# Kernel optimization log

Measured on AMD Instinct MI355X. Metric: run time of the kernel, lower is better.

Reference implementation:

```python
import jax, jax.numpy as jnp
import numpy as np

D_MODEL = 1024
NUM_HEADS = 16
HEAD_DIM = D_MODEL // NUM_HEADS
THETA = 10000.0


def _init_linear(key, d_out, d_in):
    sigma = np.sqrt(2.0 / (d_in + d_out))
    w = jax.random.truncated_normal(key, -3.0, 3.0, (d_out, d_in), dtype=jnp.float32)
    return w * sigma


def setup_inputs() -> dict:
    key = jax.random.key(0)
    kh, kq, kk, kv, ko = jax.random.split(key, 5)
    h = jax.random.normal(kh, (2, 2048, D_MODEL), dtype=jnp.float32)
    return {
        "h": h,
        "wq": _init_linear(kq, D_MODEL, D_MODEL),
        "wk": _init_linear(kk, D_MODEL, D_MODEL),
        "wv": _init_linear(kv, D_MODEL, D_MODEL),
        "wo": _init_linear(ko, D_MODEL, D_MODEL),
    }


def _rope(x, pos):
    # x: [B, H, T, dh]; rotate interleaved pairs (..., 2k, 2k+1)
    dh = x.shape[-1]
    freq = THETA ** (-jnp.arange(0, dh // 2, dtype=jnp.float32) / (dh // 2))
    ang = pos[:, None] * freq[None, :]            # [T, dh/2]
    cos, sin = jnp.cos(ang), jnp.sin(ang)
    xr = x.reshape(*x.shape[:-1], dh // 2, 2)
    x0, x1 = xr[..., 0], xr[..., 1]
    out = jnp.stack((cos * x0 - sin * x1, sin * x0 + cos * x1), axis=-1)
    return out.reshape(x.shape)


def reference(h, wq, wk, wv, wo):
    B, T, D = h.shape
    Hn, dh = NUM_HEADS, HEAD_DIM

    def split_heads(x):  # [B,T,D] -> [B,H,T,dh]
        return x.reshape(B, T, Hn, dh).transpose(0, 2, 1, 3)

    Q = split_heads(h @ wq.T)
    K = split_heads(h @ wk.T)
    V = split_heads(h @ wv.T)

    pos = jnp.arange(T, dtype=jnp.float32)
    Q = _rope(Q, pos)
    K = _rope(K, pos)

    scores = jnp.einsum('bhqd,bhkd->bhqk', Q, K) / jnp.sqrt(jnp.float32(dh))
    mask = jnp.tril(jnp.ones((T, T), dtype=bool))
    scores = jnp.where(mask, scores, -jnp.inf)
    attn = jax.nn.softmax(scores, axis=-1)
    out = jnp.einsum('bhqk,bhkd->bhqd', attn, V)   # [B,H,T,dh]
    out = out.transpose(0, 2, 1, 3).reshape(B, T, D)
    return out @ wo.T
```

## Files before the change

### kernel.cpp

```cpp
#include <hip/hip_runtime.h>
#include <math.h>

typedef __bf16 bf16_t;
typedef __bf16 v8bf __attribute__((ext_vector_type(8)));
typedef __bf16 v4bf __attribute__((ext_vector_type(4)));
typedef float  v4f  __attribute__((ext_vector_type(4)));

#define AS1 __attribute__((address_space(1)))
#define AS3 __attribute__((address_space(3)))

static __device__ __forceinline__ void load_lds16(const bf16_t* g, bf16_t* l) {
    __builtin_amdgcn_global_load_lds((AS1 void*)const_cast<bf16_t*>(g),
                                     (AS3 void*)l, 16, 0, 0);
}

static __device__ __forceinline__ void fast_sincos(float ang, float* sn, float* cs) {
    float rv = ang * 0.15915494309189535f;
    rv -= floorf(rv);
    const float a = rv * 6.283185307179586f;
    *sn = __sinf(a);
    *cs = __cosf(a);
}

__global__ __launch_bounds__(256) void cvt_fp32_bf16(
    const float* __restrict__ h,  const float* __restrict__ wq,
    const float* __restrict__ wk, const float* __restrict__ wv,
    const float* __restrict__ wo,
    bf16_t* __restrict__ hb,  bf16_t* __restrict__ wqb,
    bf16_t* __restrict__ wkb, bf16_t* __restrict__ wvb,
    bf16_t* __restrict__ wob)
{
    const size_t HM = (size_t)4 << 20;
    const size_t i8 = ((size_t)blockIdx.x * 256 + threadIdx.x) * 8;
    const float* src; bf16_t* dst; size_t off;
    if (i8 < HM) { src = h; dst = hb; off = i8; }
    else {
        const size_t r = (i8 - HM) >> 20;
        off = (i8 - HM) & (((size_t)1 << 20) - 1);
        src = (r == 0) ? wq  : (r == 1) ? wk  : (r == 2) ? wv  : wo;
        dst = (r == 0) ? wqb : (r == 1) ? wkb : (r == 2) ? wvb : wob;
    }
    const float4 a = *(const float4*)(src + off);
    const float4 b = *(const float4*)(src + off + 4);
    v8bf o;
    o[0]=(bf16_t)a.x; o[1]=(bf16_t)a.y; o[2]=(bf16_t)a.z; o[3]=(bf16_t)a.w;
    o[4]=(bf16_t)b.x; o[5]=(bf16_t)b.y; o[6]=(bf16_t)b.z; o[7]=(bf16_t)b.w;
    *(v8bf*)(dst + off) = o;
}

__global__ __launch_bounds__(256) void qkv_gemm_rope(
    const bf16_t* __restrict__ A,
    const bf16_t* __restrict__ wq,
    const bf16_t* __restrict__ wk,
    const bf16_t* __restrict__ wv,
    bf16_t* __restrict__ qo, bf16_t* __restrict__ ko, bf16_t* __restrict__ vo)
{
    __shared__ __align__(16) bf16_t smem[17408];
    bf16_t* As = smem;
    bf16_t* Bs = smem + 4096;

    const int tid = threadIdx.x;
    const int n0  = blockIdx.x * 128;
    const int m0  = blockIdx.y * 128;
    const int sel = n0 >> 10;
    const bf16_t* W = (sel == 0) ? wq : (sel == 1) ? wk : wv;
    const int wr0 = n0 & 1023;

    const int wave = tid >> 6;
    const int lane = tid & 63;
    const int l16  = lane & 15;
    const int quad = lane >> 4;
    const int wrow = (wave >> 1) * 64;
    const int wcol = (wave & 1) * 64;

    v4f acc[4][4];
    #pragma unroll
    for (int i = 0; i < 4; ++i)
        #pragma unroll
        for (int j = 0; j < 4; ++j) acc[i][j] = (v4f)(0.0f);

    for (int kt = 0; kt < 32; ++kt) {
        const int k0 = kt * 32;
        #pragma unroll
        for (int rep = 0; rep < 2; ++rep) {
            const int c   = rep * 256 + tid;
            const int row = c >> 2;
            const int col = (c & 3) * 8;
            load_lds16(A + (size_t)(m0 + row) * 1024 + k0 + col, &As[c * 8]);
            load_lds16(W + (size_t)(wr0 + row) * 1024 + k0 + col, &Bs[c * 8]);
        }
        __syncthreads();

        v8bf af[4], bfb[4];
        #pragma unroll
        for (int i = 0; i < 4; ++i) {
            af[i]  = *(const v8bf*)&As[(wrow + i * 16 + l16) * 32 + quad * 8];
            bfb[i] = *(const v8bf*)&Bs[(wcol + i * 16 + l16) * 32 + quad * 8];
        }
        #pragma unroll
        for (int i = 0; i < 4; ++i)
            #pragma unroll
            for (int j = 0; j < 4; ++j)
                acc[i][j] = __builtin_amdgcn_mfma_f32_16x16x32_bf16(
                    af[i], bfb[j], acc[i][j], 0, 0, 0);
        __syncthreads();
    }

    bf16_t* Ls = smem + wave * 4352;
    const int bq     = (m0 + wrow) >> 11;
    const int hd     = ((n0 + wcol) >> 6) & 15;
    const int t_base = (m0 + wrow) & 2047;

    if (sel < 2) {
        bf16_t* OUT = (sel == 0) ? qo : ko;
        #pragma unroll
        for (int i = 0; i < 4; ++i) {
            #pragma unroll
            for (int j = 0; j < 4; ++j) {
                #pragma unroll
                for (int r = 0; r < 4; ++r) {
                    const int mrow = i * 16 + quad * 4 + r;
                    const int dcol = j * 16 + l16;
                    float v = acc[i][j][r];
                    const float vp = __shfl_xor(v, 1);
                    const int t  = t_base + mrow;
                    const int kk = dcol >> 1;
                    const float freq = exp2f((float)kk * -0.4152410118609203f);
                    float sn, cs;
                    fast_sincos((float)t * freq, &sn, &cs);
                    v = ((dcol & 1) == 0) ? (cs * v - sn * vp) : (sn * vp + cs * v);
                    Ls[mrow * 68 + dcol] = (bf16_t)v;
                }
            }
        }
        #pragma unroll
        for (int s = 0; s < 8; ++s) {
            const int row = s * 8 + (lane >> 3);
            const int off = (lane & 7) * 8;
            const v8bf vv = *(const v8bf*)&Ls[row * 68 + off];
            *(v8bf*)(OUT + (((size_t)(bq * 16 + hd) * 2048) + t_base + row) * 64 + off) = vv;
        }
    } else {
        #pragma unroll
        for (int i = 0; i < 4; ++i)
            #pragma unroll
            for (int j = 0; j < 4; ++j) {
                v4bf p;
                #pragma unroll
                for (int r = 0; r < 4; ++r) p[r] = (bf16_t)acc[i][j][r];
                *(v4bf*)&Ls[(j * 16 + l16) * 68 + i * 16 + quad * 4] = p;
            }
        #pragma unroll
        for (int s = 0; s < 8; ++s) {
            const int drow = s * 8 + (lane >> 3);
            const int off  = (lane & 7) * 8;
            const v8bf vv = *(const v8bf*)&Ls[drow * 68 + off];
            *(v8bf*)(vo + (((size_t)(bq * 16 + hd) * 64) + drow) * 2048 + t_base + off) = vv;
        }
    }
}

__global__ __launch_bounds__(512, 4) void attn_mfma(
    const bf16_t* __restrict__ qg,
    const bf16_t* __restrict__ kg,
    const bf16_t* __restrict__ vtg,
    bf16_t* __restrict__ og)
{
    __shared__ __align__(16) bf16_t Ks[2][64 * 72];
    __shared__ __align__(16) bf16_t Vs[2][64 * 72];
    __shared__ __align__(16) bf16_t Ps[8][16 * 72];

    const int tid  = threadIdx.x;
    const int wave = tid >> 6;
    const int lane = tid & 63;
    const int l16  = lane & 15;
    const int quad = lane >> 4;

    const int i  = blockIdx.x;
    const int tt = i >> 3;
    const int u  = tt & 15;
    const int g  = tt >> 4;
    const int q128 = (((g + 1) >> 1) & 1) ? (15 - u) : u;
    const int bh = (i & 7) * 4 + g;
    const int b = bh >> 4, hh = bh & 15;

    const bf16_t* Kb = kg  + (size_t)bh * 2048 * 64;
    const bf16_t* Vb = vtg + (size_t)bh * 64 * 2048;

    const int qglb = q128 * 128 + wave * 16 + l16;
    const int diag_kt = 2 * q128 + (wave >> 2);
    const int ktmax = 2 * q128 + 1;

    const bf16_t* qrow = qg + ((size_t)bh * 2048 + qglb) * 64;
    v8bf qf[2];
    qf[0] = *(const v8bf*)(qrow + quad * 8);
    qf[1] = *(const v8bf*)(qrow + 32 + quad * 8);
    #pragma unroll
    for (int e = 0; e < 8; ++e) {
        qf[0][e] = (bf16_t)((float)qf[0][e] * 0.18033688011112042f);
        qf[1][e] = (bf16_t)((float)qf[1][e] * 0.18033688011112042f);
    }

    v8bf ones1;
    #pragma unroll
    for (int e = 0; e < 8; ++e) ones1[e] = (bf16_t)1.0f;

    float m_r = -1e30f;
    v4f l_acc = (v4f)(0.0f);
    v4f o_acc[4];
    #pragma unroll
    for (int d = 0; d < 4; ++d) o_acc[d] = (v4f)(0.0f);

    const int srow = tid >> 3;
    const int scol = (tid & 7) * 8;
    {
        const v8bf k0 = *(const v8bf*)(Kb + (size_t)srow * 64 + scol);
        const v8bf v0 = *(const v8bf*)(Vb + (size_t)srow * 2048 + scol);
        *(v8bf*)&Ks[0][srow * 72 + scol] = k0;
        *(v8bf*)&Vs[0][srow * 72 + scol] = v0;
    }

    for (int kt = 0; kt <= ktmax; ++kt) {
        const int cur = kt & 1;
        const int nxt = cur ^ 1;
        __syncthreads();

        v8bf kreg, vreg;
        if (kt < ktmax) {
            kreg = *(const v8bf*)(Kb + ((size_t)(kt + 1) * 64 + srow) * 64 + scol);
            vreg = *(const v8bf*)(Vb + (size_t)srow * 2048 + (kt + 1) * 64 + scol);
        }

        const bool active = (kt * 64) <= (q128 * 128 + wave * 16 + 15);
        if (active) {
            v4f s_acc[4];
            #pragma unroll
            for (int kblk = 0; kblk < 4; ++kblk) s_acc[kblk] = (v4f)(0.0f);
            #pragma unroll
            for (int kblk = 0; kblk < 4; ++kblk) {
                const v8bf kf0 = *(const v8bf*)&Ks[cur][(kblk * 16 + l16) * 72 + quad * 8];
                const v8bf kf1 = *(const v8bf*)&Ks[cur][(kblk * 16 + l16) * 72 + 32 + quad * 8];
                s_acc[kblk] = __builtin_amdgcn_mfma_f32_16x16x32_bf16(
                    kf0, qf[0], s_acc[kblk], 0, 0, 0);
                s_acc[kblk] = __builtin_amdgcn_mfma_f32_16x16x32_bf16(
                    kf1, qf[1], s_acc[kblk], 0, 0, 0);
            }

            if (kt == diag_kt) {
                #pragma unroll
                for (int kblk = 0; kblk < 4; ++kblk)
                    #pragma unroll
                    for (int r = 0; r < 4; ++r)
                        if (kt * 64 + kblk * 16 + quad * 4 + r > qglb)
                            s_acc[kblk][r] = -1e30f;
            }

            float mx = -1e30f;
            #pragma unroll
            for (int kblk = 0; kblk < 4; ++kblk)
                #pragma unroll
                for (int r = 0; r < 4; ++r) mx = fmaxf(mx, s_acc[kblk][r]);
            mx = fmaxf(mx, __shfl_xor(mx, 16));
            mx = fmaxf(mx, __shfl_xor(mx, 32));
            const float m_new = fmaxf(m_r, mx);
            const float alpha = exp2f(m_r - m_new);
            m_r = m_new;
            #pragma unroll
            for (int kblk = 0; kblk < 4; ++kblk)
                #pragma unroll
                for (int r = 0; r < 4; ++r)
                    s_acc[kblk][r] = exp2f(s_acc[kblk][r] - m_new);

            #pragma unroll
            for (int kblk = 0; kblk < 4; ++kblk) {
                v4bf p;
                #pragma unroll
                for (int r = 0; r < 4; ++r) p[r] = (bf16_t)s_acc[kblk][r];
                *(v4bf*)&Ps[wave][l16 * 72 + kblk * 16 + quad * 4] = p;
            }
            #pragma unroll
            for (int d = 0; d < 4; ++d) o_acc[d] *= alpha;
            l_acc *= alpha;

            const v8bf pf0 = *(const v8bf*)&Ps[wave][l16 * 72 + quad * 8];
            const v8bf pf1 = *(const v8bf*)&Ps[wave][l16 * 72 + 32 + quad * 8];
            #pragma unroll
            for (int dblk = 0; dblk < 4; ++dblk) {
                const v8bf vf0 = *(const v8bf*)&Vs[cur][(dblk * 16 + l16) * 72 + quad * 8];
                const v8bf vf1 = *(const v8bf*)&Vs[cur][(dblk * 16 + l16) * 72 + 32 + quad * 8];
                o_acc[dblk] = __builtin_amdgcn_mfma_f32_16x16x32_bf16(
                    vf0, pf0, o_acc[dblk], 0, 0, 0);
                o_acc[dblk] = __builtin_amdgcn_mfma_f32_16x16x32_bf16(
                    vf1, pf1, o_acc[dblk], 0, 0, 0);
            }
            l_acc = __builtin_amdgcn_mfma_f32_16x16x32_bf16(ones1, pf0, l_acc, 0, 0, 0);
            l_acc = __builtin_amdgcn_mfma_f32_16x16x32_bf16(ones1, pf1, l_acc, 0, 0, 0);
        }

        if (kt < ktmax) {
            *(v8bf*)&Ks[nxt][srow * 72 + scol] = kreg;
            *(v8bf*)&Vs[nxt][srow * 72 + scol] = vreg;
        }
    }

    const float inv_l = 1.0f / l_acc[0];
    const size_t base = ((size_t)b * 2048 + qglb) * 1024 + hh * 64;
    #pragma unroll
    for (int dblk = 0; dblk < 4; ++dblk) {
        v4bf o;
        #pragma unroll
        for (int r = 0; r < 4; ++r) o[r] = (bf16_t)(o_acc[dblk][r] * inv_l);
        *(v4bf*)(og + base + dblk * 16 + quad * 4) = o;
    }
}

__global__ __launch_bounds__(256) void out_gemm(
    const bf16_t* __restrict__ A,
    const bf16_t* __restrict__ W,
    float* __restrict__ C)
{
    __shared__ __align__(16) float smemf[4352];
    bf16_t* As = (bf16_t*)smemf;
    bf16_t* Bs = As + 4096;

    const int tid = threadIdx.x;
    const int n0  = blockIdx.x * 64;
    const int m0  = blockIdx.y * 128;

    const int wave = tid >> 6;
    const int lane = tid & 63;
    const int l16  = lane & 15;
    const int quad = lane >> 4;
    const int wrow = (wave >> 1) * 64;
    const int wcol = (wave & 1) * 32;

    v4f acc[4][2];
    #pragma unroll
    for (int i = 0; i < 4; ++i)
        #pragma unroll
        for (int j = 0; j < 2; ++j) acc[i][j] = (v4f)(0.0f);

    for (int kt = 0; kt < 32; ++kt) {
        const int k0 = kt * 32;
        #pragma unroll
        for (int rep = 0; rep < 2; ++rep) {
            const int c   = rep * 256 + tid;
            const int row = c >> 2;
            const int col = (c & 3) * 8;
            load_lds16(A + (size_t)(m0 + row) * 1024 + k0 + col, &As[c * 8]);
        }
        {
            const int row = tid >> 2;
            const int col = (tid & 3) * 8;
            load_lds16(W + (size_t)(n0 + row) * 1024 + k0 + col, &Bs[tid * 8]);
        }
        __syncthreads();

        v8bf af[4], bfb[2];
        #pragma unroll
        for (int i = 0; i < 4; ++i)
            af[i]  = *(const v8bf*)&As[(wrow + i * 16 + l16) * 32 + quad * 8];
        #pragma unroll
        for (int j = 0; j < 2; ++j)
            bfb[j] = *(const v8bf*)&Bs[(wcol + j * 16 + l16) * 32 + quad * 8];
        #pragma unroll
        for (int i = 0; i < 4; ++i)
            #pragma unroll
            for (int j = 0; j < 2; ++j)
                acc[i][j] = __builtin_amdgcn_mfma_f32_16x16x32_bf16(
                    af[i], bfb[j], acc[i][j], 0, 0, 0);
        __syncthreads();
    }

    float* Lw = smemf + wave * 1088;
    #pragma unroll
    for (int half = 0; half < 2; ++half) {
        #pragma unroll
        for (int ii = 0; ii < 2; ++ii) {
            const int i = half * 2 + ii;
            #pragma unroll
            for (int j = 0; j < 2; ++j)
                #pragma unroll
                for (int r = 0; r < 4; ++r)
                    Lw[(ii * 16 + quad * 4 + r) * 34 + j * 16 + l16] = acc[i][j][r];
        }
        #pragma unroll
        for (int s = 0; s < 8; ++s) {
            const int row = s * 4 + (lane >> 4);
            const float2 vv = *(const float2*)&Lw[row * 34 + l16 * 2];
            *(float2*)(C + (size_t)(m0 + wrow + half * 32 + row) * 1024
                         + n0 + wcol + l16 * 2) = vv;
        }
    }
}

extern "C" void kernel_launch(void* const* d_in, const int* in_sizes, int n_in,
                              void* d_out, int out_size, void* d_ws, size_t ws_size,
                              hipStream_t stream) {
    const float* h  = (const float*)d_in[0];
    const float* wq = (const float*)d_in[1];
    const float* wk = (const float*)d_in[2];
    const float* wv = (const float*)d_in[3];
    const float* wo = (const float*)d_in[4];

    const size_t NH = (size_t)4096 * 1024;
    const size_t NW = (size_t)1024 * 1024;

    bf16_t* hb  = (bf16_t*)d_ws;
    bf16_t* wqb = hb  + NH;
    bf16_t* wkb = wqb + NW;
    bf16_t* wvb = wkb + NW;
    bf16_t* wob = wvb + NW;
    bf16_t* qw  = wob + NW;
    bf16_t* kw  = qw + NH;
    bf16_t* vw  = kw + NH;
    bf16_t* og  = hb;

    cvt_fp32_bf16<<<dim3(4096), dim3(256), 0, stream>>>(
        h, wq, wk, wv, wo, hb, wqb, wkb, wvb, wob);
    qkv_gemm_rope<<<dim3(24, 32), dim3(256), 0, stream>>>(
        hb, wqb, wkb, wvb, qw, kw, vw);
    attn_mfma<<<dim3(512), dim3(512), 0, stream>>>(qw, kw, vw, og);
    out_gemm<<<dim3(16, 32), dim3(256), 0, stream>>>(og, wob, (float*)d_out);
}
```

Before: 184.8 us.

## Give each attention wave two query tiles, swizzle LDS, skip rescales lazily

```diff
diff --git a/kernel.cpp b/kernel.cpp
--- a/kernel.cpp
+++ b/kernel.cpp
@@ -160,15 +160,15 @@
     }
 }
 
-__global__ __launch_bounds__(512, 4) void attn_mfma(
+__global__ __launch_bounds__(256, 3) void attn_mfma(
     const bf16_t* __restrict__ qg,
     const bf16_t* __restrict__ kg,
     const bf16_t* __restrict__ vtg,
     bf16_t* __restrict__ og)
 {
-    __shared__ __align__(16) bf16_t Ks[2][64 * 72];
-    __shared__ __align__(16) bf16_t Vs[2][64 * 72];
-    __shared__ __align__(16) bf16_t Ps[8][16 * 72];
+    __shared__ __align__(16) bf16_t Ks[2][4096];
+    __shared__ __align__(16) bf16_t Vs[2][4096];
+    __shared__ __align__(16) bf16_t Ps[8][1024];
 
     const int tid  = threadIdx.x;
     const int wave = tid >> 6;
@@ -179,138 +179,193 @@
     const int i  = blockIdx.x;
     const int tt = i >> 3;
     const int u  = tt & 15;
-    const int g  = tt >> 4;
-    const int q128 = (((g + 1) >> 1) & 1) ? (15 - u) : u;
-    const int bh = (i & 7) * 4 + g;
+    const int g4 = tt >> 4;
+    const int q128 = (((g4 + 1) >> 1) & 1) ? (15 - u) : u;
+    const int bh = (i & 7) * 4 + g4;
     const int b = bh >> 4, hh = bh & 15;
 
     const bf16_t* Kb = kg  + (size_t)bh * 2048 * 64;
     const bf16_t* Vb = vtg + (size_t)bh * 64 * 2048;
 
-    const int qglb = q128 * 128 + wave * 16 + l16;
-    const int diag_kt = 2 * q128 + (wave >> 2);
-    const int ktmax = 2 * q128 + 1;
-
-    const bf16_t* qrow = qg + ((size_t)bh * 2048 + qglb) * 64;
-    v8bf qf[2];
-    qf[0] = *(const v8bf*)(qrow + quad * 8);
-    qf[1] = *(const v8bf*)(qrow + 32 + quad * 8);
-    #pragma unroll
-    for (int e = 0; e < 8; ++e) {
-        qf[0][e] = (bf16_t)((float)qf[0][e] * 0.18033688011112042f);
-        qf[1][e] = (bf16_t)((float)qf[1][e] * 0.18033688011112042f);
+    const int qrow0   = q128 * 128 + wave * 32;
+    const int ktmax_w = 2 * q128 + (wave >> 1);
+    const int ktmax_b = 2 * q128 + 1;
+
+    const int sw  = (l16 & 7) << 4;
+    const int cb0 = (quad << 4) ^ sw;
+
+    v8bf qf[2][2];
+    #pragma unroll
+    for (int g = 0; g < 2; ++g) {
+        const bf16_t* qrow = qg + ((size_t)bh * 2048 + qrow0 + g * 16 + l16) * 64;
+        qf[g][0] = *(const v8bf*)(qrow + quad * 8);
+        qf[g][1] = *(const v8bf*)(qrow + 32 + quad * 8);
+        #pragma unroll
+        for (int e = 0; e < 8; ++e) {
+            qf[g][0][e] = (bf16_t)((float)qf[g][0][e] * 0.18033688011112042f);
+            qf[g][1][e] = (bf16_t)((float)qf[g][1][e] * 0.18033688011112042f);
+        }
     }
 
     v8bf ones1;
     #pragma unroll
     for (int e = 0; e < 8; ++e) ones1[e] = (bf16_t)1.0f;
 
-    float m_r = -1e30f;
-    v4f l_acc = (v4f)(0.0f);
-    v4f o_acc[4];
-    #pragma unroll
-    for (int d = 0; d < 4; ++d) o_acc[d] = (v4f)(0.0f);
-
-    const int srow = tid >> 3;
-    const int scol = (tid & 7) * 8;
+    float m_r[2] = {-1e30f, -1e30f};
+    v4f l_acc[2];
+    l_acc[0] = (v4f)(0.0f); l_acc[1] = (v4f)(0.0f);
+    v4f o_acc[2][4];
+    #pragma unroll
+    for (int g = 0; g < 2; ++g)
+        #pragma unroll
+        for (int d = 0; d < 4; ++d) o_acc[g][d] = (v4f)(0.0f);
+
+    const int srow = tid >> 2;
+    const int sc   = (tid & 3) << 4;
+    const int swr  = (srow & 7) << 4;
+    const int sb0  = (sc * 2) ^ swr;
+    const int sb1  = (sc * 2 + 16) ^ swr;
+
     {
-        const v8bf k0 = *(const v8bf*)(Kb + (size_t)srow * 64 + scol);
-        const v8bf v0 = *(const v8bf*)(Vb + (size_t)srow * 2048 + scol);
-        *(v8bf*)&Ks[0][srow * 72 + scol] = k0;
-        *(v8bf*)&Vs[0][srow * 72 + scol] = v0;
-    }
-
-    for (int kt = 0; kt <= ktmax; ++kt) {
+        const bf16_t* kp = Kb + (size_t)srow * 64 + sc;
+        const bf16_t* vp = Vb + (size_t)srow * 2048 + sc;
+        char* kd = (char*)Ks[0] + (srow << 7);
+        char* vd = (char*)Vs[0] + (srow << 7);
+        *(v8bf*)(kd + sb0) = *(const v8bf*)kp;
+        *(v8bf*)(kd + sb1) = *(const v8bf*)(kp + 8);
+        *(v8bf*)(vd + sb0) = *(const v8bf*)vp;
+        *(v8bf*)(vd + sb1) = *(const v8bf*)(vp + 8);
+    }
+
+    for (int kt = 0; kt <= ktmax_b; ++kt) {
         const int cur = kt & 1;
         const int nxt = cur ^ 1;
         __syncthreads();
 
-        v8bf kreg, vreg;
-        if (kt < ktmax) {
-            kreg = *(const v8bf*)(Kb + ((size_t)(kt + 1) * 64 + srow) * 64 + scol);
-            vreg = *(const v8bf*)(Vb + (size_t)srow * 2048 + (kt + 1) * 64 + scol);
-        }
-
-        const bool active = (kt * 64) <= (q128 * 128 + wave * 16 + 15);
-        if (active) {
-            v4f s_acc[4];
-            #pragma unroll
-            for (int kblk = 0; kblk < 4; ++kblk) s_acc[kblk] = (v4f)(0.0f);
+        v8bf k0, k1, v0, v1;
+        if (kt < ktmax_b) {
+            const bf16_t* kp = Kb + ((size_t)(kt + 1) * 64 + srow) * 64 + sc;
+            const bf16_t* vp = Vb + (size_t)srow * 2048 + (kt + 1) * 64 + sc;
+            k0 = *(const v8bf*)kp; k1 = *(const v8bf*)(kp + 8);
+            v0 = *(const v8bf*)vp; v1 = *(const v8bf*)(vp + 8);
+        }
+
+        if (kt <= ktmax_w) {
+            const char* ksc = (const char*)Ks[cur];
+            v4f s[2][4];
+            #pragma unroll
+            for (int g = 0; g < 2; ++g)
+                #pragma unroll
+                for (int kblk = 0; kblk < 4; ++kblk) s[g][kblk] = (v4f)(0.0f);
             #pragma unroll
             for (int kblk = 0; kblk < 4; ++kblk) {
-                const v8bf kf0 = *(const v8bf*)&Ks[cur][(kblk * 16 + l16) * 72 + quad * 8];
-                const v8bf kf1 = *(const v8bf*)&Ks[cur][(kblk * 16 + l16) * 72 + 32 + quad * 8];
-                s_acc[kblk] = __builtin_amdgcn_mfma_f32_16x16x32_bf16(
-                    kf0, qf[0], s_acc[kblk], 0, 0, 0);
-                s_acc[kblk] = __builtin_amdgcn_mfma_f32_16x16x32_bf16(
-                    kf1, qf[1], s_acc[kblk], 0, 0, 0);
-            }
-
-            if (kt == diag_kt) {
+                const char* kr = ksc + ((kblk * 16 + l16) << 7);
+                const v8bf kf0 = *(const v8bf*)(kr + cb0);
+                const v8bf kf1 = *(const v8bf*)(kr + (cb0 ^ 64));
+                s[0][kblk] = __builtin_amdgcn_mfma_f32_16x16x32_bf16(
+                    kf0, qf[0][0], s[0][kblk], 0, 0, 0);
+                s[1][kblk] = __builtin_amdgcn_mfma_f32_16x16x32_bf16(
+                    kf0, qf[1][0], s[1][kblk], 0, 0, 0);
+                s[0][kblk] = __builtin_amdgcn_mfma_f32_16x16x32_bf16(
+                    kf1, qf[0][1], s[0][kblk], 0, 0, 0);
+                s[1][kblk] = __builtin_amdgcn_mfma_f32_16x16x32_bf16(
+                    kf1, qf[1][1], s[1][kblk], 0, 0, 0);
+            }
+
+            if (kt == ktmax_w) {
+                #pragma unroll
+                for (int g = 0; g < 2; ++g) {
+                    const int qglb = qrow0 + g * 16 + l16;
+                    #pragma unroll
+                    for (int kblk = 0; kblk < 4; ++kblk)
+                        #pragma unroll
+                        for (int r = 0; r < 4; ++r)
+                            if (kt * 64 + kblk * 16 + quad * 4 + r > qglb)
+                                s[g][kblk][r] = -1e30f;
+                }
+            }
+
+            #pragma unroll
+            for (int g = 0; g < 2; ++g) {
+                float mx = -1e30f;
                 #pragma unroll
                 for (int kblk = 0; kblk < 4; ++kblk)
                     #pragma unroll
+                    for (int r = 0; r < 4; ++r) mx = fmaxf(mx, s[g][kblk][r]);
+                mx = fmaxf(mx, __shfl_xor(mx, 16));
+                mx = fmaxf(mx, __shfl_xor(mx, 32));
+                if (!__all(mx - m_r[g] <= 8.0f)) {
+                    const float mn = fmaxf(m_r[g], mx);
+                    const float a  = exp2f(m_r[g] - mn);
+                    m_r[g] = mn;
+                    l_acc[g] *= a;
+                    #pragma unroll
+                    for (int d = 0; d < 4; ++d) o_acc[g][d] *= a;
+                }
+                char* psc = (char*)Ps[wave * 2 + g] + (l16 << 7);
+                #pragma unroll
+                for (int kblk = 0; kblk < 4; ++kblk) {
+                    v4bf p;
+                    #pragma unroll
                     for (int r = 0; r < 4; ++r)
-                        if (kt * 64 + kblk * 16 + quad * 4 + r > qglb)
-                            s_acc[kblk][r] = -1e30f;
-            }
-
-            float mx = -1e30f;
-            #pragma unroll
-            for (int kblk = 0; kblk < 4; ++kblk)
-                #pragma unroll
-                for (int r = 0; r < 4; ++r) mx = fmaxf(mx, s_acc[kblk][r]);
-            mx = fmaxf(mx, __shfl_xor(mx, 16));
-            mx = fmaxf(mx, __shfl_xor(mx, 32));
-            const float m_new = fmaxf(m_r, mx);
-            const float alpha = exp2f(m_r - m_new);
-            m_r = m_new;
-            #pragma unroll
-            for (int kblk = 0; kblk < 4; ++kblk)
-                #pragma unroll
-                for (int r = 0; r < 4; ++r)
-                    s_acc[kblk][r] = exp2f(s_acc[kblk][r] - m_new);
-
-            #pragma unroll
-            for (int kblk = 0; kblk < 4; ++kblk) {
-                v4bf p;
-                #pragma unroll
-                for (int r = 0; r < 4; ++r) p[r] = (bf16_t)s_acc[kblk][r];
-                *(v4bf*)&Ps[wave][l16 * 72 + kblk * 16 + quad * 4] = p;
-            }
-            #pragma unroll
-            for (int d = 0; d < 4; ++d) o_acc[d] *= alpha;
-            l_acc *= alpha;
-
-            const v8bf pf0 = *(const v8bf*)&Ps[wave][l16 * 72 + quad * 8];
-            const v8bf pf1 = *(const v8bf*)&Ps[wave][l16 * 72 + 32 + quad * 8];
+                        p[r] = (bf16_t)exp2f(s[g][kblk][r] - m_r[g]);
+                    *(v4bf*)(psc + (((kblk << 5) + (quad << 3)) ^ sw)) = p;
+                }
+            }
+
+            const char* vsc = (const char*)Vs[cur];
+            v8bf pf[2][2];
+            #pragma unroll
+            for (int g = 0; g < 2; ++g) {
+                const char* psc = (const char*)Ps[wave * 2 + g] + (l16 << 7);
+                pf[g][0] = *(const v8bf*)(psc + cb0);
+                pf[g][1] = *(const v8bf*)(psc + (cb0 ^ 64));
+            }
             #pragma unroll
             for (int dblk = 0; dblk < 4; ++dblk) {
-                const v8bf vf0 = *(const v8bf*)&Vs[cur][(dblk * 16 + l16) * 72 + quad * 8];
-                const v8bf vf1 = *(const v8bf*)&Vs[cur][(dblk * 16 + l16) * 72 + 32 + quad * 8];
-                o_acc[dblk] = __builtin_amdgcn_mfma_f32_16x16x32_bf16(
-                    vf0, pf0, o_acc[dblk], 0, 0, 0);
-                o_acc[dblk] = __builtin_amdgcn_mfma_f32_16x16x32_bf16(
-                    vf1, pf1, o_acc[dblk], 0, 0, 0);
-            }
-            l_acc = __builtin_amdgcn_mfma_f32_16x16x32_bf16(ones1, pf0, l_acc, 0, 0, 0);
-            l_acc = __builtin_amdgcn_mfma_f32_16x16x32_bf16(ones1, pf1, l_acc, 0, 0, 0);
-        }
-
-        if (kt < ktmax) {
-            *(v8bf*)&Ks[nxt][srow * 72 + scol] = kreg;
-            *(v8bf*)&Vs[nxt][srow * 72 + scol] = vreg;
-        }
-    }
-
-    const float inv_l = 1.0f / l_acc[0];
-    const size_t base = ((size_t)b * 2048 + qglb) * 1024 + hh * 64;
-    #pragma unroll
-    for (int dblk = 0; dblk < 4; ++dblk) {
-        v4bf o;
-        #pragma unroll
-        for (int r = 0; r < 4; ++r) o[r] = (bf16_t)(o_acc[dblk][r] * inv_l);
-        *(v4bf*)(og + base + dblk * 16 + quad * 4) = o;
+                const char* vr = vsc + ((dblk * 16 + l16) << 7);
+                const v8bf vf0 = *(const v8bf*)(vr + cb0);
+                const v8bf vf1 = *(const v8bf*)(vr + (cb0 ^ 64));
+                o_acc[0][dblk] = __builtin_amdgcn_mfma_f32_16x16x32_bf16(
+                    vf0, pf[0][0], o_acc[0][dblk], 0, 0, 0);
+                o_acc[1][dblk] = __builtin_amdgcn_mfma_f32_16x16x32_bf16(
+                    vf0, pf[1][0], o_acc[1][dblk], 0, 0, 0);
+                o_acc[0][dblk] = __builtin_amdgcn_mfma_f32_16x16x32_bf16(
+                    vf1, pf[0][1], o_acc[0][dblk], 0, 0, 0);
+                o_acc[1][dblk] = __builtin_amdgcn_mfma_f32_16x16x32_bf16(
+                    vf1, pf[1][1], o_acc[1][dblk], 0, 0, 0);
+            }
+            l_acc[0] = __builtin_amdgcn_mfma_f32_16x16x32_bf16(
+                ones1, pf[0][0], l_acc[0], 0, 0, 0);
+            l_acc[0] = __builtin_amdgcn_mfma_f32_16x16x32_bf16(
+                ones1, pf[0][1], l_acc[0], 0, 0, 0);
+            l_acc[1] = __builtin_amdgcn_mfma_f32_16x16x32_bf16(
+                ones1, pf[1][0], l_acc[1], 0, 0, 0);
+            l_acc[1] = __builtin_amdgcn_mfma_f32_16x16x32_bf16(
+                ones1, pf[1][1], l_acc[1], 0, 0, 0);
+        }
+
+        if (kt < ktmax_b) {
+            char* kd = (char*)Ks[nxt] + (srow << 7);
+            char* vd = (char*)Vs[nxt] + (srow << 7);
+            *(v8bf*)(kd + sb0) = k0;
+            *(v8bf*)(kd + sb1) = k1;
+            *(v8bf*)(vd + sb0) = v0;
+            *(v8bf*)(vd + sb1) = v1;
+        }
+    }
+
+    #pragma unroll
+    for (int g = 0; g < 2; ++g) {
+        const float inv_l = 1.0f / l_acc[g][0];
+        const size_t base = ((size_t)b * 2048 + qrow0 + g * 16 + l16) * 1024 + hh * 64;
+        #pragma unroll
+        for (int dblk = 0; dblk < 4; ++dblk) {
+            v4bf o;
+            #pragma unroll
+            for (int r = 0; r < 4; ++r) o[r] = (bf16_t)(o_acc[g][dblk][r] * inv_l);
+            *(v4bf*)(og + base + dblk * 16 + quad * 4) = o;
+        }
     }
 }
 
@@ -420,6 +475,6 @@
         h, wq, wk, wv, wo, hb, wqb, wkb, wvb, wob);
     qkv_gemm_rope<<<dim3(24, 32), dim3(256), 0, stream>>>(
         hb, wqb, wkb, wvb, qw, kw, vw);
-    attn_mfma<<<dim3(512), dim3(512), 0, stream>>>(qw, kw, vw, og);
+    attn_mfma<<<dim3(512), dim3(256), 0, stream>>>(qw, kw, vw, og);
     out_gemm<<<dim3(16, 32), dim3(256), 0, stream>>>(og, wob, (float*)d_out);
 }
```

Measured after the change: 191.7 us. 1.04x slower.

## Restructure attention: 64-row query tiles, async LDS loads, XOR swizzle, lazy rescale

Applied to the files above, without the earlier changes.

```diff
diff --git a/kernel.cpp b/kernel.cpp
--- a/kernel.cpp
+++ b/kernel.cpp
@@ -11,6 +11,10 @@
 
 static __device__ __forceinline__ void load_lds16(const bf16_t* g, bf16_t* l) {
     __builtin_amdgcn_global_load_lds((AS1 void*)const_cast<bf16_t*>(g),
+                                     (AS3 void*)l, 16, 0, 0);
+}
+static __device__ __forceinline__ void load_lds16b(const char* g, char* l) {
+    __builtin_amdgcn_global_load_lds((AS1 void*)const_cast<char*>(g),
                                      (AS3 void*)l, 16, 0, 0);
 }
 
@@ -160,15 +164,15 @@
     }
 }
 
-__global__ __launch_bounds__(512, 4) void attn_mfma(
+__global__ __launch_bounds__(256, 4) void attn_mfma(
     const bf16_t* __restrict__ qg,
     const bf16_t* __restrict__ kg,
     const bf16_t* __restrict__ vtg,
     bf16_t* __restrict__ og)
 {
-    __shared__ __align__(16) bf16_t Ks[2][64 * 72];
-    __shared__ __align__(16) bf16_t Vs[2][64 * 72];
-    __shared__ __align__(16) bf16_t Ps[8][16 * 72];
+    __shared__ __align__(16) bf16_t Ks[2][4096];
+    __shared__ __align__(16) bf16_t Vs[2][4096];
+    __shared__ __align__(16) bf16_t Ps[4][1024];
 
     const int tid  = threadIdx.x;
     const int wave = tid >> 6;
@@ -176,20 +180,25 @@
     const int l16  = lane & 15;
     const int quad = lane >> 4;
 
-    const int i  = blockIdx.x;
-    const int tt = i >> 3;
-    const int u  = tt & 15;
-    const int g  = tt >> 4;
-    const int q128 = (((g + 1) >> 1) & 1) ? (15 - u) : u;
-    const int bh = (i & 7) * 4 + g;
+    const int i   = blockIdx.x;
+    const int xcd = i & 7;
+    const int j   = i >> 3;
+    const int bhl = j >> 5;
+    const int u   = j & 31;
+    const int q64 = (bhl & 1) ? (31 - u) : u;
+    const int bh  = xcd * 4 + bhl;
     const int b = bh >> 4, hh = bh & 15;
 
-    const bf16_t* Kb = kg  + (size_t)bh * 2048 * 64;
-    const bf16_t* Vb = vtg + (size_t)bh * 64 * 2048;
-
-    const int qglb = q128 * 128 + wave * 16 + l16;
-    const int diag_kt = 2 * q128 + (wave >> 2);
-    const int ktmax = 2 * q128 + 1;
+    const char* Kb = (const char*)(kg  + (size_t)bh * 2048 * 64);
+    const char* Vb = (const char*)(vtg + (size_t)bh * 64 * 2048);
+
+    const int qglb = q64 * 64 + wave * 16 + l16;
+
+    const int sw  = (l16 & 7) << 4;
+    const int cb0 = (quad << 4) ^ sw;
+
+    const int grow = tid >> 3;
+    const int gsw  = ((tid & 7) << 4) ^ ((grow & 7) << 4);
 
     const bf16_t* qrow = qg + ((size_t)bh * 2048 + qglb) * 64;
     v8bf qf[2];
@@ -211,96 +220,98 @@
     #pragma unroll
     for (int d = 0; d < 4; ++d) o_acc[d] = (v4f)(0.0f);
 
-    const int srow = tid >> 3;
-    const int scol = (tid & 7) * 8;
     {
-        const v8bf k0 = *(const v8bf*)(Kb + (size_t)srow * 64 + scol);
-        const v8bf v0 = *(const v8bf*)(Vb + (size_t)srow * 2048 + scol);
-        *(v8bf*)&Ks[0][srow * 72 + scol] = k0;
-        *(v8bf*)&Vs[0][srow * 72 + scol] = v0;
-    }
-
-    for (int kt = 0; kt <= ktmax; ++kt) {
+        const char* ks = Kb + ((size_t)grow << 7) + gsw;
+        const char* vs = Vb + ((size_t)grow << 12) + gsw;
+        char* kd = (char*)Ks[0] + tid * 16;
+        char* vd = (char*)Vs[0] + tid * 16;
+        load_lds16b(ks, kd);
+        load_lds16b(ks + (32 << 7), kd + 4096);
+        load_lds16b(vs, vd);
+        load_lds16b(vs + ((size_t)32 << 12), vd + 4096);
+    }
+
+    for (int kt = 0; kt <= q64; ++kt) {
         const int cur = kt & 1;
         const int nxt = cur ^ 1;
         __syncthreads();
 
-        v8bf kreg, vreg;
-        if (kt < ktmax) {
-            kreg = *(const v8bf*)(Kb + ((size_t)(kt + 1) * 64 + srow) * 64 + scol);
-            vreg = *(const v8bf*)(Vb + (size_t)srow * 2048 + (kt + 1) * 64 + scol);
-        }
-
-        const bool active = (kt * 64) <= (q128 * 128 + wave * 16 + 15);
-        if (active) {
-            v4f s_acc[4];
-            #pragma unroll
-            for (int kblk = 0; kblk < 4; ++kblk) s_acc[kblk] = (v4f)(0.0f);
-            #pragma unroll
-            for (int kblk = 0; kblk < 4; ++kblk) {
-                const v8bf kf0 = *(const v8bf*)&Ks[cur][(kblk * 16 + l16) * 72 + quad * 8];
-                const v8bf kf1 = *(const v8bf*)&Ks[cur][(kblk * 16 + l16) * 72 + 32 + quad * 8];
-                s_acc[kblk] = __builtin_amdgcn_mfma_f32_16x16x32_bf16(
-                    kf0, qf[0], s_acc[kblk], 0, 0, 0);
-                s_acc[kblk] = __builtin_amdgcn_mfma_f32_16x16x32_bf16(
-                    kf1, qf[1], s_acc[kblk], 0, 0, 0);
-            }
-
-            if (kt == diag_kt) {
-                #pragma unroll
-                for (int kblk = 0; kblk < 4; ++kblk)
-                    #pragma unroll
-                    for (int r = 0; r < 4; ++r)
-                        if (kt * 64 + kblk * 16 + quad * 4 + r > qglb)
-                            s_acc[kblk][r] = -1e30f;
-            }
-
-            float mx = -1e30f;
-            #pragma unroll
-            for (int kblk = 0; kblk < 4; ++kblk)
-                #pragma unroll
-                for (int r = 0; r < 4; ++r) mx = fmaxf(mx, s_acc[kblk][r]);
-            mx = fmaxf(mx, __shfl_xor(mx, 16));
-            mx = fmaxf(mx, __shfl_xor(mx, 32));
-            const float m_new = fmaxf(m_r, mx);
-            const float alpha = exp2f(m_r - m_new);
-            m_r = m_new;
+        if (kt < q64) {
+            const char* ks = Kb + ((size_t)((kt + 1) * 64 + grow) << 7) + gsw;
+            const char* vs = Vb + ((size_t)grow << 12) + ((size_t)(kt + 1) << 7) + gsw;
+            char* kd = (char*)Ks[nxt] + tid * 16;
+            char* vd = (char*)Vs[nxt] + tid * 16;
+            load_lds16b(ks, kd);
+            load_lds16b(ks + (32 << 7), kd + 4096);
+            load_lds16b(vs, vd);
+            load_lds16b(vs + ((size_t)32 << 12), vd + 4096);
+        }
+
+        const char* ksc = (const char*)Ks[cur];
+        v4f s_acc[4];
+        #pragma unroll
+        for (int kblk = 0; kblk < 4; ++kblk) s_acc[kblk] = (v4f)(0.0f);
+        #pragma unroll
+        for (int kblk = 0; kblk < 4; ++kblk) {
+            const char* kr = ksc + ((kblk * 16 + l16) << 7);
+            const v8bf kf0 = *(const v8bf*)(kr + cb0);
+            const v8bf kf1 = *(const v8bf*)(kr + (cb0 ^ 64));
+            s_acc[kblk] = __builtin_amdgcn_mfma_f32_16x16x32_bf16(
+                kf0, qf[0], s_acc[kblk], 0, 0, 0);
+            s_acc[kblk] = __builtin_amdgcn_mfma_f32_16x16x32_bf16(
+                kf1, qf[1], s_acc[kblk], 0, 0, 0);
+        }
+
+        if (kt == q64) {
             #pragma unroll
             for (int kblk = 0; kblk < 4; ++kblk)
                 #pragma unroll
                 for (int r = 0; r < 4; ++r)
-                    s_acc[kblk][r] = exp2f(s_acc[kblk][r] - m_new);
-
-            #pragma unroll
-            for (int kblk = 0; kblk < 4; ++kblk) {
-                v4bf p;
-                #pragma unroll
-                for (int r = 0; r < 4; ++r) p[r] = (bf16_t)s_acc[kblk][r];
-                *(v4bf*)&Ps[wave][l16 * 72 + kblk * 16 + quad * 4] = p;
-            }
-            #pragma unroll
-            for (int d = 0; d < 4; ++d) o_acc[d] *= alpha;
-            l_acc *= alpha;
-
-            const v8bf pf0 = *(const v8bf*)&Ps[wave][l16 * 72 + quad * 8];
-            const v8bf pf1 = *(const v8bf*)&Ps[wave][l16 * 72 + 32 + quad * 8];
-            #pragma unroll
-            for (int dblk = 0; dblk < 4; ++dblk) {
-                const v8bf vf0 = *(const v8bf*)&Vs[cur][(dblk * 16 + l16) * 72 + quad * 8];
-                const v8bf vf1 = *(const v8bf*)&Vs[cur][(dblk * 16 + l16) * 72 + 32 + quad * 8];
-                o_acc[dblk] = __builtin_amdgcn_mfma_f32_16x16x32_bf16(
-                    vf0, pf0, o_acc[dblk], 0, 0, 0);
-                o_acc[dblk] = __builtin_amdgcn_mfma_f32_16x16x32_bf16(
-                    vf1, pf1, o_acc[dblk], 0, 0, 0);
-            }
-            l_acc = __builtin_amdgcn_mfma_f32_16x16x32_bf16(ones1, pf0, l_acc, 0, 0, 0);
-            l_acc = __builtin_amdgcn_mfma_f32_16x16x32_bf16(ones1, pf1, l_acc, 0, 0, 0);
-        }
-
-        if (kt < ktmax) {
-            *(v8bf*)&Ks[nxt][srow * 72 + scol] = kreg;
-            *(v8bf*)&Vs[nxt][srow * 72 + scol] = vreg;
-        }
+                    if (kt * 64 + kblk * 16 + quad * 4 + r > qglb)
+                        s_acc[kblk][r] = -1e30f;
+        }
+
+        float mx = -1e30f;
+        #pragma unroll
+        for (int kblk = 0; kblk < 4; ++kblk)
+            #pragma unroll
+            for (int r = 0; r < 4; ++r) mx = fmaxf(mx, s_acc[kblk][r]);
+        mx = fmaxf(mx, __shfl_xor(mx, 16));
+        mx = fmaxf(mx, __shfl_xor(mx, 32));
+        if (!__all(mx - m_r <= 8.0f)) {
+            const float mn = fmaxf(m_r, mx);
+            const float a  = exp2f(m_r - mn);
+            m_r = mn;
+            l_acc *= a;
+            #pragma unroll
+            for (int d = 0; d < 4; ++d) o_acc[d] *= a;
+        }
+
+        char* psc = (char*)Ps[wave] + (l16 << 7);
+        #pragma unroll
+        for (int kblk = 0; kblk < 4; ++kblk) {
+            v4bf p;
+            #pragma unroll
+            for (int r = 0; r < 4; ++r)
+                p[r] = (bf16_t)exp2f(s_acc[kblk][r] - m_r);
+            *(v4bf*)(psc + ((kblk * 32 + quad * 8) ^ sw)) = p;
+        }
+        const v8bf pf0 = *(const v8bf*)(psc + cb0);
+        const v8bf pf1 = *(const v8bf*)(psc + (cb0 ^ 64));
+
+        const char* vsc = (const char*)Vs[cur];
+        #pragma unroll
+        for (int dblk = 0; dblk < 4; ++dblk) {
+            const char* vr = vsc + ((dblk * 16 + l16) << 7);
+            const v8bf vf0 = *(const v8bf*)(vr + cb0);
+            const v8bf vf1 = *(const v8bf*)(vr + (cb0 ^ 64));
+            o_acc[dblk] = __builtin_amdgcn_mfma_f32_16x16x32_bf16(
+                vf0, pf0, o_acc[dblk], 0, 0, 0);
+            o_acc[dblk] = __builtin_amdgcn_mfma_f32_16x16x32_bf16(
+                vf1, pf1, o_acc[dblk], 0, 0, 0);
+        }
+        l_acc = __builtin_amdgcn_mfma_f32_16x16x32_bf16(ones1, pf0, l_acc, 0, 0, 0);
+        l_acc = __builtin_amdgcn_mfma_f32_16x16x32_bf16(ones1, pf1, l_acc, 0, 0, 0);
     }
 
     const float inv_l = 1.0f / l_acc[0];
@@ -420,6 +431,6 @@
         h, wq, wk, wv, wo, hb, wqb, wkb, wvb, wob);
     qkv_gemm_rope<<<dim3(24, 32), dim3(256), 0, stream>>>(
         hb, wqb, wkb, wvb, qw, kw, vw);
-    attn_mfma<<<dim3(512), dim3(512), 0, stream>>>(qw, kw, vw, og);
+    attn_mfma<<<dim3(1024), dim3(256), 0, stream>>>(qw, kw, vw, og);
     out_gemm<<<dim3(16, 32), dim3(256), 0, stream>>>(og, wob, (float*)d_out);
 }
```

New measurement: 187.9 us. Within noise of the previous version (+1.7%).
